# Kernel optimization log

Hardware: AMD Instinct MI355X
Metric: run time of the kernel (lower is better)

The kernel has to match this reference:

```python
import jax, jax.numpy as jnp
import numpy as np

P = 113
VOCAB = P + 2  # 115
EMB = 128
HID = 512


def setup_inputs() -> dict:
    key = jax.random.key(0)
    ks = jax.random.split(key, 7)
    k = HID ** 0.5
    X = jax.random.randint(ks[0], (1024, 256), 0, VOCAB)
    W_emb = jax.random.normal(ks[1], (VOCAB, EMB), dtype=jnp.float32)
    W_xh = jax.random.normal(ks[2], (EMB, HID), dtype=jnp.float32) / k
    W_hh = jax.random.normal(ks[3], (HID, HID), dtype=jnp.float32) / k
    b_h = jnp.zeros((HID,), dtype=jnp.float32)
    W_hy = jax.random.normal(ks[4], (HID, VOCAB), dtype=jnp.float32) / k
    b_y = jnp.zeros((VOCAB,), dtype=jnp.float32)
    return {"X": X, "W_emb": W_emb, "W_xh": W_xh, "W_hh": W_hh,
            "b_h": b_h, "W_hy": W_hy, "b_y": b_y}


def reference(X, W_emb, W_xh, W_hh, b_h, W_hy, b_y):
    # Embed: [B, T, E]
    emb = W_emb[X]
    B = emb.shape[0]
    # Precompute input projection for all timesteps: [T, B, H]
    xh = jnp.einsum("bte,eh->tbh", emb, W_xh)

    def step(h, xh_t):
        h = jnp.tanh(xh_t + h @ W_hh + b_h)
        return h, None

    h0 = jnp.zeros((B, HID), dtype=emb.dtype)
    h_T, _ = jax.lax.scan(step, h0, xh)
    logits = h_T @ W_hy + b_y  # [B, VOCAB]
    return logits
```

## Files before the change

### kernel.cpp

```cpp
#include <hip/hip_runtime.h>


typedef __attribute__((ext_vector_type(4))) float f32x4;
typedef __attribute__((ext_vector_type(8))) _Float16 f16x8;

#define T_ 256
#define E_ 128
#define H_ 512
#define V_ 115

__device__ __forceinline__ float tanh_fast(float x) {
  float e = __builtin_exp2f(x * 2.8853900817779268f);
  return 1.0f - 2.0f * __builtin_amdgcn_rcpf(e + 1.0f);
}

__device__ __forceinline__ void sync_lgkm() {
  asm volatile("s_waitcnt lgkmcnt(0)" ::: "memory");
  __builtin_amdgcn_s_barrier();
}

__global__ void prep_table(const float* __restrict__ Wemb, const float* __restrict__ Wxh,
                           const float* __restrict__ bh, float* __restrict__ Txh) {
  int v = blockIdx.x;
  int h = threadIdx.x;
  float s = bh[h];
  const float* we = Wemb + v * E_;
#pragma unroll 8
  for (int e = 0; e < E_; ++e) s += we[e] * Wxh[e * H_ + h];
  Txh[v * H_ + h] = s;
}

__global__ void prep_wf(const float* __restrict__ Whh, _Float16* __restrict__ Wf) {
  int idx = blockIdx.x * 256 + threadIdx.x;
  int k = idx >> 9, n = idx & 511;
  float w = Whh[k * H_ + n];
  int nb = n >> 4, lm = n & 15, kc = k >> 5, lg = (k >> 3) & 3, kk = k & 7;
  Wf[(((nb * 16 + kc) * 4 + lg) * 16 + lm) * 8 + kk] = (_Float16)w;
}

#define WG(f, s) (((const f16x8*)Wf)[(((nb0 + (f)) * 16 + (s)) << 6) + lane])

#define DECL2(s) f16x8 W##s##_0 = WG(0, s), W##s##_1 = WG(1, s);
#define PIN2(s)  asm volatile("" : "+a"(W##s##_0), "+a"(W##s##_1));

#define MMB(ac, a8, wv) \
  ac = __builtin_amdgcn_mfma_f32_16x16x32_f16(a8, wv, ac, 0, 0, 0);

#define RSET(s) {                                                  \
  f16x8 a8 = *(const f16x8*)(acur + (s) * 512 + lane * 8);         \
  MMB(acc0, a8, W##s##_0) MMB(acc1, a8, W##s##_1) }

#define SSET(buf, s) {                                             \
  f16x8 a8 = *(const f16x8*)(acur + (s) * 512 + lane * 8);         \
  MMB(acc0, a8, buf[0]) MMB(acc1, a8, buf[1]) }
#define SLOAD(buf, s) { buf[0] = WG(0, s); buf[1] = WG(1, s); }

#define LSET(j) {                                                  \
  f16x8 a8 = *(const f16x8*)(acur + (12 + (j)) * 512 + lane * 8);  \
  const f16x8* wp = (const f16x8*)WL + ((w * 8 + (j) * 2) << 6) + lane; \
  f16x8 q0 = wp[0], q1 = wp[64];                                   \
  MMB(acc0, a8, q0) MMB(acc1, a8, q1) }

#define EPI(f) {                                                   \
  int n = w * 32 + (f) * 16 + lm;                                  \
  int bidx = (n >> 5) * 512 + ((n >> 3) & 3) * 128 + (n & 7);      \
  _Pragma("unroll")                                                \
  for (int r = 0; r < 4; ++r) {                                    \
    float hv = tanh_fast(acc##f[r]);                               \
    anxt[bidx + (lg * 4 + r) * 8] = (_Float16)hv;                  \
  } }

__global__ __launch_bounds__(1024, 4)
void rnn_main(const int* __restrict__ X, const float* __restrict__ Txh,
              const _Float16* __restrict__ Wf, const float* __restrict__ Why,
              const float* __restrict__ by, float* __restrict__ out) {
  __shared__ _Float16 Ah[2][16 * H_];
  __shared__ _Float16 WL[65536];

  const int tid = threadIdx.x;
  const int lane = tid & 63;
  const int w = tid >> 6;
  const int nb0 = w * 2;
  const int r0 = blockIdx.x * 16;
  const int lm = lane & 15;
  const int lg = lane >> 4;

  for (int i = tid; i < 16 * H_ / 2; i += 1024) ((int*)Ah[0])[i] = 0;
  for (int i = tid; i < 8192; i += 1024) {
    int bi = i >> 6, ln = i & 63;
    int w8 = bi >> 3, rem = bi & 7, j = rem >> 1, f = rem & 1;
    int nb = w8 * 2 + f;
    ((f16x8*)WL)[(bi << 6) + ln] =
        ((const f16x8*)Wf)[((nb * 16 + 12 + j) << 6) + ln];
  }

  DECL2(0) DECL2(1) DECL2(2) DECL2(3) DECL2(4) DECL2(5)
  PIN2(0) PIN2(1) PIN2(2) PIN2(3) PIN2(4) PIN2(5)

  f16x8 sa[2], sb[2];
  SLOAD(sa, 6)
  SLOAD(sb, 7)

  const float* txl = Txh + w * 32 + lm;
  const int* xrow = X + (r0 + lg * 4) * T_;

  int vx0 = xrow[0 * T_], vx1 = xrow[1 * T_], vx2 = xrow[2 * T_], vx3 = xrow[3 * T_];

  const _Float16* acur = Ah[0];
  _Float16* anxt = Ah[1];

  __syncthreads();

  for (int t = 0; t < T_; ++t) {
    f32x4 acc0, acc1;
    {
      const float* g0 = txl + vx0 * H_;
      const float* g1 = txl + vx1 * H_;
      const float* g2 = txl + vx2 * H_;
      const float* g3 = txl + vx3 * H_;
      acc0[0]=g0[0];  acc0[1]=g1[0];  acc0[2]=g2[0];  acc0[3]=g3[0];
      acc1[0]=g0[16]; acc1[1]=g1[16]; acc1[2]=g2[16]; acc1[3]=g3[16];
    }
    {
      int tn = (t + 1) & (T_ - 1);
      vx0 = xrow[tn];
      vx1 = xrow[1 * T_ + tn];
      vx2 = xrow[2 * T_ + tn];
      vx3 = xrow[3 * T_ + tn];
    }

    SSET(sa, 6)   SLOAD(sa, 8)
    SSET(sb, 7)   SLOAD(sb, 9)

    RSET(0) RSET(1) RSET(2) RSET(3) RSET(4) RSET(5)

    SSET(sa, 8)   SLOAD(sa, 10)
    SSET(sb, 9)   SLOAD(sb, 11)

    LSET(0) LSET(1)

    SSET(sa, 10)  SLOAD(sa, 6)
    SSET(sb, 11)  SLOAD(sb, 7)

    LSET(2) LSET(3)

    EPI(0) EPI(1)

    sync_lgkm();

    const _Float16* tmp = acur; acur = anxt; anxt = (_Float16*)tmp;
  }

  for (int idx = tid; idx < 16 * V_; idx += 1024) {
    int m = idx / V_, v = idx - m * V_;
    float s = by[v];
#pragma unroll 8
    for (int k = 0; k < H_; ++k) {
      float hk = (float)Ah[0][(k >> 5) * 512 + ((k >> 3) & 3) * 128 + (k & 7) + m * 8];
      s += hk * Why[k * V_ + v];
    }
    out[(r0 + m) * V_ + v] = s;
  }
}

extern "C" void kernel_launch(void* const* d_in, const int* in_sizes, int n_in,
                              void* d_out, int out_size, void* d_ws, size_t ws_size,
                              hipStream_t stream) {
  const int* X = (const int*)d_in[0];
  const float* Wemb = (const float*)d_in[1];
  const float* Wxh = (const float*)d_in[2];
  const float* Whh = (const float*)d_in[3];
  const float* bh = (const float*)d_in[4];
  const float* Why = (const float*)d_in[5];
  const float* by = (const float*)d_in[6];
  float* out = (float*)d_out;

  char* ws = (char*)d_ws;
  float* Txh = (float*)ws;
  _Float16* Wf = (_Float16*)(ws + 256 * 1024);

  prep_table<<<dim3(V_), dim3(H_), 0, stream>>>(Wemb, Wxh, bh, Txh);
  prep_wf<<<dim3(1024), dim3(256), 0, stream>>>(Whh, Wf);
  rnn_main<<<dim3(64), dim3(1024), 0, stream>>>(X, Txh, Wf, Why, by, out);
}
```

Before: 630.2 us.

## Rebalance W_hh slices across registers, streamed global loads and LDS

Each wave now pins 8 W_hh k-slices in registers instead of 6. It streams slices 8–14 from global memory through the double-buffered sa/sb pipeline, and keeps only slice 15 in LDS instead of slices 12–15. The LDS staging buffer shrinks to a quarter of its size, and per-step LDS weight reads drop. The four per-row token indices are packed into one register to free VGPRs for the extra pinned weights. In exchange each step issues more global/L2 weight loads, and register pressure from the extra pinned slices rises.

```diff
diff --git a/kernel.cpp b/kernel.cpp
--- a/kernel.cpp
+++ b/kernel.cpp
@@ -55,9 +55,9 @@
   MMB(acc0, a8, buf[0]) MMB(acc1, a8, buf[1]) }
 #define SLOAD(buf, s) { buf[0] = WG(0, s); buf[1] = WG(1, s); }
 
-#define LSET(j) {                                                  \
-  f16x8 a8 = *(const f16x8*)(acur + (12 + (j)) * 512 + lane * 8);  \
-  const f16x8* wp = (const f16x8*)WL + ((w * 8 + (j) * 2) << 6) + lane; \
+#define LSET15 {                                                   \
+  f16x8 a8 = *(const f16x8*)(acur + 15 * 512 + lane * 8);          \
+  const f16x8* wp = (const f16x8*)WL + ((w * 2) << 6) + lane;      \
   f16x8 q0 = wp[0], q1 = wp[64];                                   \
   MMB(acc0, a8, q0) MMB(acc1, a8, q1) }
 
@@ -75,7 +75,7 @@
               const _Float16* __restrict__ Wf, const float* __restrict__ Why,
               const float* __restrict__ by, float* __restrict__ out) {
   __shared__ _Float16 Ah[2][16 * H_];
-  __shared__ _Float16 WL[65536];
+  __shared__ _Float16 WL[16384];
 
   const int tid = threadIdx.x;
   const int lane = tid & 63;
@@ -86,25 +86,26 @@
   const int lg = lane >> 4;
 
   for (int i = tid; i < 16 * H_ / 2; i += 1024) ((int*)Ah[0])[i] = 0;
-  for (int i = tid; i < 8192; i += 1024) {
+  for (int i = tid; i < 2048; i += 1024) {
     int bi = i >> 6, ln = i & 63;
-    int w8 = bi >> 3, rem = bi & 7, j = rem >> 1, f = rem & 1;
+    int w8 = bi >> 1, f = bi & 1;
     int nb = w8 * 2 + f;
     ((f16x8*)WL)[(bi << 6) + ln] =
-        ((const f16x8*)Wf)[((nb * 16 + 12 + j) << 6) + ln];
+        ((const f16x8*)Wf)[((nb * 16 + 15) << 6) + ln];
   }
 
-  DECL2(0) DECL2(1) DECL2(2) DECL2(3) DECL2(4) DECL2(5)
-  PIN2(0) PIN2(1) PIN2(2) PIN2(3) PIN2(4) PIN2(5)
+  DECL2(0) DECL2(1) DECL2(2) DECL2(3) DECL2(4) DECL2(5) DECL2(6) DECL2(7)
+  PIN2(0) PIN2(1) PIN2(2) PIN2(3) PIN2(4) PIN2(5) PIN2(6) PIN2(7)
 
   f16x8 sa[2], sb[2];
-  SLOAD(sa, 6)
-  SLOAD(sb, 7)
+  SLOAD(sa, 8)
+  SLOAD(sb, 9)
 
   const float* txl = Txh + w * 32 + lm;
   const int* xrow = X + (r0 + lg * 4) * T_;
 
-  int vx0 = xrow[0 * T_], vx1 = xrow[1 * T_], vx2 = xrow[2 * T_], vx3 = xrow[3 * T_];
+  int vpack = (xrow[0] & 255) | ((xrow[T_] & 255) << 8) |
+              ((xrow[2 * T_] & 255) << 16) | ((xrow[3 * T_] & 255) << 24);
 
   const _Float16* acur = Ah[0];
   _Float16* anxt = Ah[1];
@@ -114,35 +115,32 @@
   for (int t = 0; t < T_; ++t) {
     f32x4 acc0, acc1;
     {
-      const float* g0 = txl + vx0 * H_;
-      const float* g1 = txl + vx1 * H_;
-      const float* g2 = txl + vx2 * H_;
-      const float* g3 = txl + vx3 * H_;
+      const float* g0 = txl + (vpack & 255) * H_;
+      const float* g1 = txl + ((vpack >> 8) & 255) * H_;
+      const float* g2 = txl + ((vpack >> 16) & 255) * H_;
+      const float* g3 = txl + ((unsigned)vpack >> 24) * H_;
       acc0[0]=g0[0];  acc0[1]=g1[0];  acc0[2]=g2[0];  acc0[3]=g3[0];
       acc1[0]=g0[16]; acc1[1]=g1[16]; acc1[2]=g2[16]; acc1[3]=g3[16];
     }
     {
       int tn = (t + 1) & (T_ - 1);
-      vx0 = xrow[tn];
-      vx1 = xrow[1 * T_ + tn];
-      vx2 = xrow[2 * T_ + tn];
-      vx3 = xrow[3 * T_ + tn];
+      vpack = (xrow[tn] & 255) | ((xrow[T_ + tn] & 255) << 8) |
+              ((xrow[2 * T_ + tn] & 255) << 16) | ((xrow[3 * T_ + tn] & 255) << 24);
     }
-
-    SSET(sa, 6)   SLOAD(sa, 8)
-    SSET(sb, 7)   SLOAD(sb, 9)
-
-    RSET(0) RSET(1) RSET(2) RSET(3) RSET(4) RSET(5)
 
     SSET(sa, 8)   SLOAD(sa, 10)
     SSET(sb, 9)   SLOAD(sb, 11)
 
-    LSET(0) LSET(1)
+    RSET(0) RSET(1) RSET(2) RSET(3) RSET(4) RSET(5) RSET(6) RSET(7)
 
-    SSET(sa, 10)  SLOAD(sa, 6)
-    SSET(sb, 11)  SLOAD(sb, 7)
+    SSET(sa, 10)  SLOAD(sa, 12)
+    SSET(sb, 11)  SLOAD(sb, 13)
 
-    LSET(2) LSET(3)
+    LSET15
+
+    SSET(sa, 12)  SLOAD(sa, 14)
+    SSET(sb, 13)  SLOAD(sb, 9)
+    SSET(sa, 14)  SLOAD(sa, 8)
 
     EPI(0) EPI(1)
 
```

New measurement: 1.192 ms. 89.1% more time.
